# Kernel tuning notes

Measured on AMD Instinct MI355X. Metric: run time of the kernel, lower is better.

Reference implementation:

```python
import jax, jax.numpy as jnp
import numpy as np

B, NUM_CAMS, C, N_ANCHOR = 1, 6, 256, 900
NUM_LEVELS, NUM_FIXED, NUM_LEARN, NUM_GROUPS = 4, 7, 6, 8
NUM_PTS = NUM_FIXED + NUM_LEARN
IMG_W, IMG_H = 704, 256
SHAPES = [(64, 176), (32, 88), (16, 44), (8, 22)]  # strides 4,8,16,32


def setup_inputs() -> dict:
    key = jax.random.key(0)
    ks = jax.random.split(key, 12)
    sum_hw = sum(h * w for h, w in SHAPES)
    feature = jax.random.normal(ks[0], (B, NUM_CAMS, sum_hw, C), jnp.float32)
    spatial_shapes = jnp.array(SHAPES, dtype=jnp.int32)
    starts = np.cumsum([0] + [h * w for h, w in SHAPES[:-1]])
    level_start_index = jnp.array(starts, dtype=jnp.int32)
    # anchor: [x,y,z, log(w),log(l),log(h), sin(yaw), cos(yaw), vx,vy,vz]
    center = jax.random.uniform(ks[1], (B, N_ANCHOR, 3), minval=-40.0, maxval=40.0) * jnp.array([1.0, 1.0, 0.05])
    size = jnp.log(jnp.array([2.0, 4.5, 1.7])) * jnp.ones((B, N_ANCHOR, 3))
    yaw = jax.random.uniform(ks[2], (B, N_ANCHOR, 1), minval=-np.pi, maxval=np.pi)
    anchor = jnp.concatenate([center, size, jnp.sin(yaw), jnp.cos(yaw), jnp.zeros((B, N_ANCHOR, 3))], axis=-1).astype(jnp.float32)
    instance_feature = jax.random.normal(ks[3], (B, N_ANCHOR, C), jnp.float32)
    time_interval = jnp.full((B,), 0.5, jnp.float32)
    # plausible lidar2img = K @ [R|t] for 6 surround cameras
    l2i = []
    for c in range(NUM_CAMS):
        a = 2.0 * np.pi * c / NUM_CAMS
        Rz = np.array([[np.cos(a), -np.sin(a), 0.0], [np.sin(a), np.cos(a), 0.0], [0.0, 0.0, 1.0]])
        swap = np.array([[0.0, -1.0, 0.0], [0.0, 0.0, -1.0], [1.0, 0.0, 0.0]])  # lidar axes -> camera axes
        Rcam = swap @ Rz.T
        t = -Rcam @ np.array([0.0, 0.0, 1.5])
        E = np.eye(4); E[:3, :3] = Rcam; E[:3, 3] = t
        K = np.eye(4); K[0, 0] = K[1, 1] = 400.0; K[0, 2] = IMG_W / 2.0; K[1, 2] = IMG_H / 2.0
        l2i.append(K @ E)
    lidar2img = jnp.asarray(np.broadcast_to(np.stack(l2i)[None], (B, NUM_CAMS, 4, 4)), jnp.float32)
    image_wh = jnp.broadcast_to(jnp.array([IMG_W, IMG_H], jnp.float32), (B, NUM_CAMS, 2))
    s = 0.02
    n_w = NUM_CAMS * NUM_LEVELS * NUM_PTS * NUM_GROUPS
    return dict(
        instance_feature=instance_feature, anchor=anchor, time_interval=time_interval,
        feature=feature, spatial_shapes=spatial_shapes, level_start_index=level_start_index,
        lidar2img=lidar2img, image_wh=image_wh,
        enc_w=jax.random.normal(ks[4], (11, C)) * s, enc_b=jnp.zeros((C,), jnp.float32),
        kp_fixed=jax.random.normal(ks[5], (NUM_FIXED, 3)) * 0.5,
        kp_w=jax.random.normal(ks[6], (C, NUM_LEARN * 3)) * s, kp_b=jnp.zeros((NUM_LEARN * 3,), jnp.float32),
        wfc_w=jax.random.normal(ks[7], (C, n_w)) * s, wfc_b=jnp.zeros((n_w,), jnp.float32),
        out_w=jax.random.normal(ks[8], (C, C)) * s, out_b=jnp.zeros((C,), jnp.float32),
    )


def _bilinear_sample(feature, spatial_shapes, level_start_index, pts, valid):
    # feature: [B,Cm,sumHW,C]; pts: [B,Cm,N,P,2] normalized to [0,1]; valid: [B,Cm,N,P]
    Bn, Cm, _, Cd = feature.shape
    N, P = pts.shape[2], pts.shape[3]
    per_level = []
    for l in range(NUM_LEVELS):
        H = spatial_shapes[l, 0]
        W = spatial_shapes[l, 1]
        start = level_start_index[l]
        # grid_sample align_corners=False convention
        x = pts[..., 0] * W - 0.5
        y = pts[..., 1] * H - 0.5
        x0f = jnp.floor(x); y0f = jnp.floor(y)
        wx = (x - x0f)[..., None]
        wy = (y - y0f)[..., None]
        x0 = x0f.astype(jnp.int32); y0 = y0f.astype(jnp.int32)

        def gather(xi, yi):
            ok = (xi >= 0) & (xi < W) & (yi >= 0) & (yi < H) & valid
            xi_c = jnp.clip(xi, 0, W - 1)
            yi_c = jnp.clip(yi, 0, H - 1)
            idx = (start + yi_c * W + xi_c).reshape(Bn, Cm, N * P, 1)
            g = jnp.take_along_axis(feature, idx, axis=2).reshape(Bn, Cm, N, P, Cd)
            return g * ok[..., None]

        v = (gather(x0, y0) * (1 - wx) * (1 - wy)
             + gather(x0 + 1, y0) * wx * (1 - wy)
             + gather(x0, y0 + 1) * (1 - wx) * wy
             + gather(x0 + 1, y0 + 1) * wx * wy)
        per_level.append(v)
    return jnp.stack(per_level, axis=4)  # [B,Cm,N,P,L,C]


def _forward(instance_feature, anchor, feature, spatial_shapes, level_start_index,
             lidar2img, image_wh, enc_w, enc_b, kp_fixed, kp_w, kp_b, wfc_w, wfc_b, out_w, out_b):
    Bn, N, Cd = instance_feature.shape
    anchor_embed = anchor @ enc_w + enc_b                      # anchor_encoder
    # --- keypoint generation (7 fixed + 6 learnable), scaled by box size, rotated by yaw ---
    center = anchor[..., :3]
    size = jnp.exp(anchor[..., 3:6])
    sin_y, cos_y = anchor[..., 6:7], anchor[..., 7:8]
    learn = (instance_feature @ kp_w + kp_b).reshape(Bn, N, NUM_LEARN, 3)
    offs = jnp.concatenate([jnp.broadcast_to(kp_fixed, (Bn, N, NUM_FIXED, 3)), learn], axis=2)
    offs = offs * size[:, :, None, :]
    ox, oy, oz = offs[..., 0], offs[..., 1], offs[..., 2]
    rx = cos_y * ox - sin_y * oy
    ry = sin_y * ox + cos_y * oy
    kp = jnp.stack([rx, ry, oz], axis=-1) + center[:, :, None, :]          # [B,N,P,3]
    # --- project to each camera ---
    kp_h = jnp.concatenate([kp, jnp.ones_like(kp[..., :1])], axis=-1)
    p = jnp.einsum('bcij,bnpj->bcnpi', lidar2img, kp_h)                    # [B,Cm,N,P,4]
    depth = p[..., 2]
    xy = p[..., :2] / jnp.clip(depth, 1e-5, None)[..., None]
    pts = xy / image_wh[:, :, None, None, :]                               # [0,1] normalized
    valid = depth > 1e-5
    # --- multi-scale multi-camera bilinear gather ---
    feats = _bilinear_sample(feature, spatial_shapes, level_start_index, pts, valid)  # [B,Cm,N,P,L,C]
    # --- group-wise attention weights, softmax over cams*levels*pts ---
    w = ((instance_feature + anchor_embed) @ wfc_w + wfc_b).reshape(Bn, N, -1, NUM_GROUPS)
    w = jax.nn.softmax(w, axis=-2).reshape(Bn, N, NUM_CAMS, NUM_LEVELS, NUM_PTS, NUM_GROUPS)
    f = jnp.transpose(feats, (0, 2, 1, 4, 3, 5)).reshape(
        Bn, N, NUM_CAMS, NUM_LEVELS, NUM_PTS, NUM_GROUPS, Cd // NUM_GROUPS)
    agg = jnp.sum(f * w[..., None], axis=(2, 3, 4)).reshape(Bn, N, Cd)
    return instance_feature + (agg @ out_w + out_b)


def reference(instance_feature, anchor, time_interval, feature, spatial_shapes, level_start_index,
              lidar2img, image_wh, enc_w, enc_b, kp_fixed, kp_w, kp_b, wfc_w, wfc_b, out_w, out_b):
    # time_interval is only consumed by the 'refine' op, which is not in the executed op list
    return _forward(instance_feature, anchor, feature, spatial_shapes, level_start_index,
                    lidar2img, image_wh, enc_w, enc_b, kp_fixed, kp_w, kp_b, wfc_w, wfc_b, out_w, out_b)
```

## Files before the change

kernel.cpp:

```cpp
#include <hip/hip_runtime.h>
#include <math.h>

#define N_ANCHOR   900
#define NUM_CAMS   6
#define CDIM       256
#define NUM_LEVELS 4
#define NUM_FIXED  7
#define NUM_LEARN  6
#define NUM_PTS    13
#define NUM_GROUPS 8
#define NW         2496
#define NI         312
#define SUM_HW     14960
#define MAXJOBS    1248
#define PADJOBS    1280
#define WSTRIDE    328

typedef short short8 __attribute__((ext_vector_type(8)));
typedef float floatx4 __attribute__((ext_vector_type(4)));

__device__ __forceinline__ unsigned short f2bf(float x) {
  unsigned u = __float_as_uint(x);
  u += 0x7FFFu + ((u >> 16) & 1u);
  return (unsigned short)(u >> 16);
}

__global__ __launch_bounds__(256) void k_pre(
    const float* __restrict__ inst, const float* __restrict__ anchor,
    const float* __restrict__ l2i, const float* __restrict__ image_wh,
    const float* __restrict__ kp_fixed, const float* __restrict__ kp_w,
    const float* __restrict__ kp_b,
    const float* __restrict__ enc_w, const float* __restrict__ enc_b,
    const float* __restrict__ wfc_w, const float* __restrict__ out_w,
    unsigned short* __restrict__ qbf, unsigned short* __restrict__ wbf_t,
    unsigned short* __restrict__ owt,
    float* __restrict__ pts_out, float* __restrict__ valid_out) {
  const int t = threadIdx.x;

  if (blockIdx.x >= N_ANCHOR) {
    const int bi = blockIdx.x - N_ANCHOR;
    const float* src; unsigned short* dst; int ss, n0, k0;
    if (bi < 156) { src = wfc_w; dst = wbf_t; ss = NW;   n0 = (bi % 39) * 64; k0 = (bi / 39) * 64; }
    else { const int b2 = bi - 156; src = out_w; dst = owt; ss = CDIM; n0 = (b2 % 4) * 64; k0 = (b2 / 4) * 64; }
    __shared__ float tile[64][65];
    #pragma unroll
    for (int i = 0; i < 4; ++i) {
      const int kr = (t >> 4) + i * 16;
      const int nc = (t & 15) * 4;
      const float4 v = *(const float4*)&src[(size_t)(k0 + kr) * ss + n0 + nc];
      tile[kr][nc + 0] = v.x; tile[kr][nc + 1] = v.y;
      tile[kr][nc + 2] = v.z; tile[kr][nc + 3] = v.w;
    }
    __syncthreads();
    #pragma unroll
    for (int i = 0; i < 4; ++i) {
      const int nr = (t >> 4) + i * 16;
      const int kc = (t & 15) * 4;
      ushort4 o;
      o.x = f2bf(tile[kc + 0][nr]);
      o.y = f2bf(tile[kc + 1][nr]);
      o.z = f2bf(tile[kc + 2][nr]);
      o.w = f2bf(tile[kc + 3][nr]);
      *(ushort4*)&dst[(size_t)(n0 + nr) * CDIM + k0 + kc] = o;
    }
    return;
  }

  const int n = blockIdx.x;
  __shared__ float anc[11];
  __shared__ float learn[NUM_LEARN * 3];
  __shared__ float psum[8][NUM_LEARN * 3];
  __shared__ float kps[NUM_PTS][3];
  __shared__ float ins[CDIM];

  const float iv = inst[n * CDIM + t];
  ins[t] = iv;
  if (t < 11) anc[t] = anchor[n * 11 + t];
  __syncthreads();

  {
    float s = enc_b[t] + iv;
    #pragma unroll
    for (int k = 0; k < 11; ++k) s += anc[k] * enc_w[k * CDIM + t];
    qbf[n * CDIM + t] = f2bf(s);
  }

  if (t < 144) {
    const int c = t / 18, j = t % 18;
    float s = 0.0f;
    const int k0 = c * 32;
    #pragma unroll
    for (int k = 0; k < 32; ++k)
      s += ins[k0 + k] * kp_w[(k0 + k) * (NUM_LEARN * 3) + j];
    psum[c][j] = s;
  }
  __syncthreads();
  if (t < NUM_LEARN * 3) {
    float s = kp_b[t];
    #pragma unroll
    for (int c = 0; c < 8; ++c) s += psum[c][t];
    learn[t] = s;
  }
  __syncthreads();

  if (t < NUM_PTS) {
    const float sx = expf(anc[3]), sy = expf(anc[4]), sz = expf(anc[5]);
    float ox, oy, oz;
    if (t < NUM_FIXED) {
      ox = kp_fixed[t * 3 + 0]; oy = kp_fixed[t * 3 + 1]; oz = kp_fixed[t * 3 + 2];
    } else {
      const int j = (t - NUM_FIXED) * 3;
      ox = learn[j + 0]; oy = learn[j + 1]; oz = learn[j + 2];
    }
    ox *= sx; oy *= sy; oz *= sz;
    const float sn = anc[6], cs = anc[7];
    kps[t][0] = cs * ox - sn * oy + anc[0];
    kps[t][1] = sn * ox + cs * oy + anc[1];
    kps[t][2] = oz + anc[2];
  }
  __syncthreads();

  if (t < NUM_CAMS * NUM_PTS) {
    const int cam = t / NUM_PTS, p = t % NUM_PTS;
    const float* M = l2i + cam * 16;
    const float kx = kps[p][0], ky = kps[p][1], kz = kps[p][2];
    const float px = M[0] * kx + M[1] * ky + M[2]  * kz + M[3];
    const float py = M[4] * kx + M[5] * ky + M[6]  * kz + M[7];
    const float pz = M[8] * kx + M[9] * ky + M[10] * kz + M[11];
    const float d = fmaxf(pz, 1e-5f);
    const float u = (px / d) / image_wh[cam * 2 + 0];
    const float v = (py / d) / image_wh[cam * 2 + 1];
    const int o = n * NUM_CAMS * NUM_PTS + t;
    pts_out[o * 2 + 0] = u;
    pts_out[o * 2 + 1] = v;
    valid_out[o] = (pz > 1e-5f) ? 1.0f : 0.0f;
  }
}

__global__ __launch_bounds__(256) void k_wgemm(
    const unsigned short* __restrict__ qbf,
    const unsigned short* __restrict__ wbf_t,
    const float* __restrict__ wfc_b, float* __restrict__ raw) {
  const int tid = threadIdx.x;
  const int w = tid >> 6;
  const int l = tid & 63;
  const int n0 = blockIdx.x * 64;
  const int m0 = blockIdx.y * 64;
  __shared__ unsigned short Bs[64 * 64];

  floatx4 acc[4];
  #pragma unroll
  for (int s = 0; s < 4; ++s) acc[s] = (floatx4){0.f, 0.f, 0.f, 0.f};

  const int arow = m0 + w * 16 + (l & 15);
  const bool arow_ok = arow < N_ANCHOR;
  const unsigned short* aptr = qbf + (size_t)arow * CDIM + (l >> 4) * 8;

  for (int k0 = 0; k0 < CDIM; k0 += 64) {
    #pragma unroll
    for (int i = 0; i < 2; ++i) {
      const int idx = tid + i * 256;
      const int n = idx >> 3, kg = idx & 7;
      const short8 bv =
          *(const short8*)&wbf_t[(size_t)(n0 + n) * CDIM + k0 + kg * 8];
      *(short8*)&Bs[n * 64 + ((kg ^ (n & 7)) * 8)] = bv;
    }
    __syncthreads();
    #pragma unroll
    for (int c = 0; c < 2; ++c) {
      short8 a = (short8){0, 0, 0, 0, 0, 0, 0, 0};
      if (arow_ok) a = *(const short8*)&aptr[k0 + c * 32];
      #pragma unroll
      for (int s = 0; s < 4; ++s) {
        const int nloc = s * 16 + (l & 15);
        const int k8 = c * 4 + (l >> 4);
        const short8 b = *(const short8*)&Bs[nloc * 64 + ((k8 ^ (nloc & 7)) * 8)];
        acc[s] = __builtin_amdgcn_mfma_f32_16x16x32_bf16(a, b, acc[s], 0, 0, 0);
      }
    }
    __syncthreads();
  }

  const int colb = n0 + (l & 15);
  const int rowb = m0 + w * 16 + (l >> 4) * 4;
  #pragma unroll
  for (int s = 0; s < 4; ++s) {
    const int col = colb + s * 16;
    const float bias = wfc_b[col];
    #pragma unroll
    for (int r = 0; r < 4; ++r) {
      const int row = rowb + r;
      if (row < N_ANCHOR)
        raw[(size_t)row * NW + col] = acc[s][r] + bias;
    }
  }
}

__global__ __launch_bounds__(512) void k_mega(
    const float* __restrict__ feature,
    const int* __restrict__ spatial_shapes, const int* __restrict__ level_start,
    const float* __restrict__ pts, const float* __restrict__ valid,
    const float* __restrict__ raw,
    unsigned short* __restrict__ abf) {
  const int n = blockIdx.x;
  const int t = threadIdx.x;
  const int wv = t >> 6;
  const int lane = t & 63;
  const int g = lane >> 3;

  __shared__ float w_rowT[NUM_GROUPS * WSTRIDE];
  __shared__ float uv_s[NUM_CAMS * NUM_PTS][2];
  __shared__ float val_s[NUM_CAMS * NUM_PTS];
  __shared__ float mx_s[NUM_GROUPS], inv_s[NUM_GROUPS];
  __shared__ int shp[NUM_LEVELS][2];
  __shared__ int lst[NUM_LEVELS];
  __shared__ int joff[PADJOBS];
  __shared__ float jcf[PADJOBS];
  __shared__ short jw_s[PADJOBS];
  __shared__ int njobs;
  __shared__ float4 red4[8][64];

  {
    const float4* src = (const float4*)(raw + (size_t)n * NW);
    for (int j4 = t; j4 < NW / 4; j4 += 512) {
      const float4 v = src[j4];
      const int i = j4 >> 1;
      const int gb = (j4 & 1) * 4;
      w_rowT[(gb + 0) * WSTRIDE + i] = v.x;
      w_rowT[(gb + 1) * WSTRIDE + i] = v.y;
      w_rowT[(gb + 2) * WSTRIDE + i] = v.z;
      w_rowT[(gb + 3) * WSTRIDE + i] = v.w;
    }
  }
  if (t < NUM_CAMS * NUM_PTS) {
    const int o = n * NUM_CAMS * NUM_PTS + t;
    uv_s[t][0] = pts[o * 2 + 0];
    uv_s[t][1] = pts[o * 2 + 1];
    val_s[t] = valid[o];
  }
  if (t < NUM_LEVELS) {
    shp[t][0] = spatial_shapes[t * 2 + 0];
    shp[t][1] = spatial_shapes[t * 2 + 1];
    lst[t] = level_start[t];
  }
  if (t == 0) njobs = 0;
  __syncthreads();

  {
    const float* wr = &w_rowT[wv * WSTRIDE];
    float m = -1e30f;
    for (int i = lane; i < NI; i += 64) m = fmaxf(m, wr[i]);
    #pragma unroll
    for (int o = 32; o > 0; o >>= 1) m = fmaxf(m, __shfl_down(m, o, 64));
    m = __shfl(m, 0, 64);
    float s = 0.0f;
    for (int i = lane; i < NI; i += 64) s += expf(wr[i] - m);
    #pragma unroll
    for (int o = 32; o > 0; o >>= 1) s += __shfl_down(s, o, 64);
    if (lane == 0) { mx_s[wv] = m; inv_s[wv] = 1.0f / s; }
  }

  #pragma unroll
  for (int base = 0; base < MAXJOBS; base += 512) {
    const int jt = base + t;
    bool ok = false;
    int off = 0; short wbi = 0; float cf = 0.0f;
    if (jt < MAXJOBS) {
      const int cam = jt / 208;
      const int r = jt % 208;
      const int q = r / 52;
      const int pl = r % 52;
      const int p = pl >> 2, l = pl & 3;
      if (val_s[cam * NUM_PTS + p] != 0.0f) {
        const int H = shp[l][0], W = shp[l][1], st = lst[l];
        const float x = uv_s[cam * NUM_PTS + p][0] * (float)W - 0.5f;
        const float y = uv_s[cam * NUM_PTS + p][1] * (float)H - 0.5f;
        const float x0f = floorf(x), y0f = floorf(y);
        const float wx = x - x0f, wy = y - y0f;
        const int dx = q & 1, dy = q >> 1;
        const int xx = (int)x0f + dx;
        const int yy = (int)y0f + dy;
        if (xx >= 0 && xx < W && yy >= 0 && yy < H) {
          ok = true;
          off = (cam * SUM_HW + st + yy * W + xx) * CDIM;
          cf = (dx ? wx : 1.0f - wx) * (dy ? wy : 1.0f - wy);
          wbi = (short)(cam * 52 + l * NUM_PTS + p);
        }
      }
    }
    const unsigned long long mask = __ballot(ok);
    const int cnt = __popcll(mask);
    int wbase = 0;
    if (lane == 0 && cnt) wbase = atomicAdd(&njobs, cnt);
    wbase = __shfl(wbase, 0, 64);
    if (ok) {
      const int pos = wbase + __popcll(mask & ((1ull << lane) - 1ull));
      joff[pos] = off; jcf[pos] = cf; jw_s[pos] = wbi;
    }
  }
  __syncthreads();

  const int nj = njobs;
  const int padded = (nj + 63) & ~63;
  for (int j = nj + t; j < padded; j += 512) {
    joff[j] = 0; jcf[j] = 0.0f; jw_s[j] = 0;
  }
  for (int e = t; e < NUM_GROUPS * WSTRIDE; e += 512) {
    const int gg = e / WSTRIDE;
    w_rowT[e] = expf(w_rowT[e] - mx_s[gg]) * inv_s[gg];
  }
  __syncthreads();

  float4 acc = make_float4(0.f, 0.f, 0.f, 0.f);
  const int cio = lane * 4;
  const float* wgrp = &w_rowT[g * WSTRIDE];
  for (int j = wv; j < padded; j += 64) {
    float4 f[8]; float wg[8];
    #pragma unroll
    for (int i = 0; i < 8; ++i) {
      const int jj = j + i * 8;
      const int o = joff[jj];
      wg[i] = jcf[jj] * wgrp[jw_s[jj]];
      f[i] = *(const float4*)&feature[o + cio];
    }
    #pragma unroll
    for (int i = 0; i < 8; ++i) {
      acc.x += wg[i] * f[i].x; acc.y += wg[i] * f[i].y;
      acc.z += wg[i] * f[i].z; acc.w += wg[i] * f[i].w;
    }
  }
  red4[wv][lane] = acc;
  __syncthreads();

  if (t < 64) {
    float4 s = red4[0][t];
    #pragma unroll
    for (int w = 1; w < 8; ++w) {
      const float4 b = red4[w][t];
      s.x += b.x; s.y += b.y; s.z += b.z; s.w += b.w;
    }
    ushort4 o;
    o.x = f2bf(s.x); o.y = f2bf(s.y); o.z = f2bf(s.z); o.w = f2bf(s.w);
    *(ushort4*)&abf[(size_t)n * CDIM + t * 4] = o;
  }
}

__global__ __launch_bounds__(256) void k_ogemm(
    const unsigned short* __restrict__ abf,
    const unsigned short* __restrict__ owt,
    const float* __restrict__ out_b, const float* __restrict__ inst,
    float* __restrict__ out) {
  const int tid = threadIdx.x;
  const int w = tid >> 6;
  const int l = tid & 63;
  const int n0 = blockIdx.x * 64;
  const int m0 = blockIdx.y * 64;
  __shared__ unsigned short Bs[64 * 64];

  floatx4 acc[4];
  #pragma unroll
  for (int s = 0; s < 4; ++s) acc[s] = (floatx4){0.f, 0.f, 0.f, 0.f};

  const int arow = m0 + w * 16 + (l & 15);
  const bool arow_ok = arow < N_ANCHOR;
  const unsigned short* aptr = abf + (size_t)arow * CDIM + (l >> 4) * 8;

  for (int k0 = 0; k0 < CDIM; k0 += 64) {
    #pragma unroll
    for (int i = 0; i < 2; ++i) {
      const int idx = tid + i * 256;
      const int n = idx >> 3, kg = idx & 7;
      const short8 bv =
          *(const short8*)&owt[(size_t)(n0 + n) * CDIM + k0 + kg * 8];
      *(short8*)&Bs[n * 64 + ((kg ^ (n & 7)) * 8)] = bv;
    }
    __syncthreads();
    #pragma unroll
    for (int c = 0; c < 2; ++c) {
      short8 a = (short8){0, 0, 0, 0, 0, 0, 0, 0};
      if (arow_ok) a = *(const short8*)&aptr[k0 + c * 32];
      #pragma unroll
      for (int s = 0; s < 4; ++s) {
        const int nloc = s * 16 + (l & 15);
        const int k8 = c * 4 + (l >> 4);
        const short8 b = *(const short8*)&Bs[nloc * 64 + ((k8 ^ (nloc & 7)) * 8)];
        acc[s] = __builtin_amdgcn_mfma_f32_16x16x32_bf16(a, b, acc[s], 0, 0, 0);
      }
    }
    __syncthreads();
  }

  const int colb = n0 + (l & 15);
  const int rowb = m0 + w * 16 + (l >> 4) * 4;
  #pragma unroll
  for (int s = 0; s < 4; ++s) {
    const int col = colb + s * 16;
    const float bias = out_b[col];
    #pragma unroll
    for (int r = 0; r < 4; ++r) {
      const int row = rowb + r;
      if (row < N_ANCHOR)
        out[(size_t)row * CDIM + col] =
            acc[s][r] + bias + inst[(size_t)row * CDIM + col];
    }
  }
}

extern "C" void kernel_launch(void* const* d_in, const int* in_sizes, int n_in,
                              void* d_out, int out_size, void* d_ws, size_t ws_size,
                              hipStream_t stream) {
  const float* inst           = (const float*)d_in[0];
  const float* anchor         = (const float*)d_in[1];
  const float* feature        = (const float*)d_in[3];
  const int*   spatial_shapes = (const int*)d_in[4];
  const int*   level_start    = (const int*)d_in[5];
  const float* l2i            = (const float*)d_in[6];
  const float* image_wh       = (const float*)d_in[7];
  const float* enc_w          = (const float*)d_in[8];
  const float* enc_b          = (const float*)d_in[9];
  const float* kp_fixed       = (const float*)d_in[10];
  const float* kp_w           = (const float*)d_in[11];
  const float* kp_b           = (const float*)d_in[12];
  const float* wfc_w          = (const float*)d_in[13];
  const float* wfc_b          = (const float*)d_in[14];
  const float* out_w          = (const float*)d_in[15];
  const float* out_b          = (const float*)d_in[16];

  float* ws    = (float*)d_ws;
  float* pts   = ws;
  float* valid = pts + N_ANCHOR * NUM_CAMS * NUM_PTS * 2;
  float* wbuf  = valid + N_ANCHOR * NUM_CAMS * NUM_PTS;
  unsigned short* qbf   = (unsigned short*)(wbuf + (size_t)N_ANCHOR * NW);
  unsigned short* wbf_t = qbf + N_ANCHOR * CDIM;
  unsigned short* owt   = wbf_t + (size_t)NW * CDIM;
  unsigned short* abf   = owt + CDIM * CDIM;

  k_pre<<<N_ANCHOR + 156 + 16, 256, 0, stream>>>(
      inst, anchor, l2i, image_wh, kp_fixed, kp_w, kp_b, enc_w, enc_b,
      wfc_w, out_w, qbf, wbf_t, owt, pts, valid);
  k_wgemm<<<dim3(NW / 64, (N_ANCHOR + 63) / 64), 256, 0, stream>>>(
      qbf, wbf_t, wfc_b, wbuf);
  k_mega<<<N_ANCHOR, 512, 0, stream>>>(
      feature, spatial_shapes, level_start, pts, valid, wbuf, abf);
  k_ogemm<<<dim3(CDIM / 64, (N_ANCHOR + 63) / 64), 256, 0, stream>>>(
      abf, owt, out_b, inst, (float*)d_out);
}
```

Measured before the change: 196.8 us.

## Fuse output projection into gather kernel, drop separate bf16 output GEMM

The final output projection GEMM is moved into the tail of the per-anchor gather kernel. Each block now computes its own 256-wide row as an fp32 matvec against out_w, reading from shared memory, and adds bias and residual. This removes one kernel launch, the bf16 intermediate write and read, and the out_w transpose blocks in the pre kernel. In exchange, every one of the 900 blocks re-reads the full 256x256 fp32 out_w from global or L2, using scalar FMAs instead of MFMA.

Measured after the change: 198.4 us. No clear change (+0.8%).

```diff
diff --git a/kernel.cpp b/kernel.cpp
--- a/kernel.cpp
+++ b/kernel.cpp
@@ -31,23 +31,20 @@
     const float* __restrict__ kp_fixed, const float* __restrict__ kp_w,
     const float* __restrict__ kp_b,
     const float* __restrict__ enc_w, const float* __restrict__ enc_b,
-    const float* __restrict__ wfc_w, const float* __restrict__ out_w,
+    const float* __restrict__ wfc_w,
     unsigned short* __restrict__ qbf, unsigned short* __restrict__ wbf_t,
-    unsigned short* __restrict__ owt,
     float* __restrict__ pts_out, float* __restrict__ valid_out) {
   const int t = threadIdx.x;
 
   if (blockIdx.x >= N_ANCHOR) {
     const int bi = blockIdx.x - N_ANCHOR;
-    const float* src; unsigned short* dst; int ss, n0, k0;
-    if (bi < 156) { src = wfc_w; dst = wbf_t; ss = NW;   n0 = (bi % 39) * 64; k0 = (bi / 39) * 64; }
-    else { const int b2 = bi - 156; src = out_w; dst = owt; ss = CDIM; n0 = (b2 % 4) * 64; k0 = (b2 / 4) * 64; }
+    const int n0 = (bi % 39) * 64, k0 = (bi / 39) * 64;
     __shared__ float tile[64][65];
     #pragma unroll
     for (int i = 0; i < 4; ++i) {
       const int kr = (t >> 4) + i * 16;
       const int nc = (t & 15) * 4;
-      const float4 v = *(const float4*)&src[(size_t)(k0 + kr) * ss + n0 + nc];
+      const float4 v = *(const float4*)&wfc_w[(size_t)(k0 + kr) * NW + n0 + nc];
       tile[kr][nc + 0] = v.x; tile[kr][nc + 1] = v.y;
       tile[kr][nc + 2] = v.z; tile[kr][nc + 3] = v.w;
     }
@@ -61,7 +58,7 @@
       o.y = f2bf(tile[kc + 1][nr]);
       o.z = f2bf(tile[kc + 2][nr]);
       o.w = f2bf(tile[kc + 3][nr]);
-      *(ushort4*)&dst[(size_t)(n0 + nr) * CDIM + k0 + kc] = o;
+      *(ushort4*)&wbf_t[(size_t)(n0 + nr) * CDIM + k0 + kc] = o;
     }
     return;
   }
@@ -201,7 +198,9 @@
     const int* __restrict__ spatial_shapes, const int* __restrict__ level_start,
     const float* __restrict__ pts, const float* __restrict__ valid,
     const float* __restrict__ raw,
-    unsigned short* __restrict__ abf) {
+    const float* __restrict__ out_w, const float* __restrict__ out_b,
+    const float* __restrict__ inst,
+    float* __restrict__ out) {
   const int n = blockIdx.x;
   const int t = threadIdx.x;
   const int wv = t >> 6;
@@ -219,6 +218,8 @@
   __shared__ short jw_s[PADJOBS];
   __shared__ int njobs;
   __shared__ float4 red4[8][64];
+  __shared__ float agg_s[CDIM];
+  __shared__ float half_s[2][CDIM];
 
   {
     const float4* src = (const float4*)(raw + (size_t)n * NW);
@@ -339,70 +340,25 @@
       const float4 b = red4[w][t];
       s.x += b.x; s.y += b.y; s.z += b.z; s.w += b.w;
     }
-    ushort4 o;
-    o.x = f2bf(s.x); o.y = f2bf(s.y); o.z = f2bf(s.z); o.w = f2bf(s.w);
-    *(ushort4*)&abf[(size_t)n * CDIM + t * 4] = o;
-  }
-}
-
-__global__ __launch_bounds__(256) void k_ogemm(
-    const unsigned short* __restrict__ abf,
-    const unsigned short* __restrict__ owt,
-    const float* __restrict__ out_b, const float* __restrict__ inst,
-    float* __restrict__ out) {
-  const int tid = threadIdx.x;
-  const int w = tid >> 6;
-  const int l = tid & 63;
-  const int n0 = blockIdx.x * 64;
-  const int m0 = blockIdx.y * 64;
-  __shared__ unsigned short Bs[64 * 64];
-
-  floatx4 acc[4];
-  #pragma unroll
-  for (int s = 0; s < 4; ++s) acc[s] = (floatx4){0.f, 0.f, 0.f, 0.f};
-
-  const int arow = m0 + w * 16 + (l & 15);
-  const bool arow_ok = arow < N_ANCHOR;
-  const unsigned short* aptr = abf + (size_t)arow * CDIM + (l >> 4) * 8;
-
-  for (int k0 = 0; k0 < CDIM; k0 += 64) {
-    #pragma unroll
-    for (int i = 0; i < 2; ++i) {
-      const int idx = tid + i * 256;
-      const int n = idx >> 3, kg = idx & 7;
-      const short8 bv =
-          *(const short8*)&owt[(size_t)(n0 + n) * CDIM + k0 + kg * 8];
-      *(short8*)&Bs[n * 64 + ((kg ^ (n & 7)) * 8)] = bv;
-    }
-    __syncthreads();
-    #pragma unroll
-    for (int c = 0; c < 2; ++c) {
-      short8 a = (short8){0, 0, 0, 0, 0, 0, 0, 0};
-      if (arow_ok) a = *(const short8*)&aptr[k0 + c * 32];
-      #pragma unroll
-      for (int s = 0; s < 4; ++s) {
-        const int nloc = s * 16 + (l & 15);
-        const int k8 = c * 4 + (l >> 4);
-        const short8 b = *(const short8*)&Bs[nloc * 64 + ((k8 ^ (nloc & 7)) * 8)];
-        acc[s] = __builtin_amdgcn_mfma_f32_16x16x32_bf16(a, b, acc[s], 0, 0, 0);
-      }
-    }
-    __syncthreads();
-  }
-
-  const int colb = n0 + (l & 15);
-  const int rowb = m0 + w * 16 + (l >> 4) * 4;
-  #pragma unroll
-  for (int s = 0; s < 4; ++s) {
-    const int col = colb + s * 16;
-    const float bias = out_b[col];
-    #pragma unroll
-    for (int r = 0; r < 4; ++r) {
-      const int row = rowb + r;
-      if (row < N_ANCHOR)
-        out[(size_t)row * CDIM + col] =
-            acc[s][r] + bias + inst[(size_t)row * CDIM + col];
-    }
+    agg_s[t * 4 + 0] = s.x; agg_s[t * 4 + 1] = s.y;
+    agg_s[t * 4 + 2] = s.z; agg_s[t * 4 + 3] = s.w;
+  }
+  __syncthreads();
+
+  {
+    const int c = t & 255, kh = t >> 8;
+    const float* owp = out_w + (size_t)(kh * 128) * CDIM + c;
+    const float* ap = agg_s + kh * 128;
+    float s = 0.0f;
+    #pragma unroll 8
+    for (int k = 0; k < 128; ++k)
+      s = fmaf(ap[k], owp[(size_t)k * CDIM], s);
+    half_s[kh][c] = s;
+  }
+  __syncthreads();
+  if (t < CDIM) {
+    out[(size_t)n * CDIM + t] =
+        half_s[0][t] + half_s[1][t] + out_b[t] + inst[(size_t)n * CDIM + t];
   }
 }
 
@@ -432,16 +388,13 @@
   float* wbuf  = valid + N_ANCHOR * NUM_CAMS * NUM_PTS;
   unsigned short* qbf   = (unsigned short*)(wbuf + (size_t)N_ANCHOR * NW);
   unsigned short* wbf_t = qbf + N_ANCHOR * CDIM;
-  unsigned short* owt   = wbf_t + (size_t)NW * CDIM;
-  unsigned short* abf   = owt + CDIM * CDIM;
-
-  k_pre<<<N_ANCHOR + 156 + 16, 256, 0, stream>>>(
+
+  k_pre<<<N_ANCHOR + 156, 256, 0, stream>>>(
       inst, anchor, l2i, image_wh, kp_fixed, kp_w, kp_b, enc_w, enc_b,
-      wfc_w, out_w, qbf, wbf_t, owt, pts, valid);
+      wfc_w, qbf, wbf_t, pts, valid);
   k_wgemm<<<dim3(NW / 64, (N_ANCHOR + 63) / 64), 256, 0, stream>>>(
       qbf, wbf_t, wfc_b, wbuf);
   k_mega<<<N_ANCHOR, 512, 0, stream>>>(
-      feature, spatial_shapes, level_start, pts, valid, wbuf, abf);
-  k_ogemm<<<dim3(CDIM / 64, (N_ANCHOR + 63) / 64), 256, 0, stream>>>(
-      abf, owt, out_b, inst, (float*)d_out);
+      feature, spatial_shapes, level_start, pts, valid, wbuf,
+      out_w, out_b, inst, (float*)d_out);
 }
```
